# Performance work log

Hardware: AMD Instinct MI355X
Metric: run time of the kernel (lower is better)

Reference implementation:

```python
import jax, jax.numpy as jnp
import numpy as np

NEG_SLOPE = 0.2  # PyG GATConv default leaky_relu slope

def _glorot(key, shape):
    fan_in, fan_out = shape[0], shape[1]
    lim = jnp.sqrt(6.0 / (fan_in + fan_out))
    return jax.random.uniform(key, shape, jnp.float32, -lim, lim)

def setup_inputs() -> dict:
    key = jax.random.key(0)
    ks = jax.random.split(key, 16)
    N, E, S = 20000, 640000, 32
    in_dim, hid, out = 384, 128, 64
    inp = {
        'persona_x': jax.random.normal(ks[0], (N, in_dim), jnp.float32),
        'persona_edge_index': jax.random.randint(ks[1], (2, E), 0, N, jnp.int64),
        'story_x': jax.random.normal(ks[2], (S, N, in_dim), jnp.float32),
        'story_edge_index': jax.random.randint(ks[3], (S, 2, E), 0, N, jnp.int64),
    }
    # persona GAT params
    inp['p_W1'] = _glorot(ks[4], (in_dim, hid)); inp['p_a1'] = _glorot(ks[5], (2 * hid, 1)).reshape(2 * hid)
    inp['p_b1'] = jnp.zeros((hid,), jnp.float32)
    inp['p_W2'] = _glorot(ks[6], (hid, out)); inp['p_a2'] = _glorot(ks[7], (2 * out, 1)).reshape(2 * out)
    inp['p_b2'] = jnp.zeros((out,), jnp.float32)
    # story GAT params
    inp['s_W1'] = _glorot(ks[8], (in_dim, hid)); inp['s_a1'] = _glorot(ks[9], (2 * hid, 1)).reshape(2 * hid)
    inp['s_b1'] = jnp.zeros((hid,), jnp.float32)
    inp['s_W2'] = _glorot(ks[10], (hid, out)); inp['s_a2'] = _glorot(ks[11], (2 * out, 1)).reshape(2 * out)
    inp['s_b2'] = jnp.zeros((out,), jnp.float32)
    inp['temperature'] = jnp.asarray(0.07, jnp.float32)
    return inp

def gat_conv(x, edge_index, W, a, b):
    # x: [N, F_in], edge_index: [2, E] (row 0 = src, row 1 = dst), PyG GATConv heads=1
    N = x.shape[0]
    h = x @ W  # [N, F_out]
    src, dst = edge_index[0], edge_index[1]
    F_out = h.shape[1]
    # PyG adds self-loops by default
    loops = jnp.arange(N, dtype=src.dtype)
    src = jnp.concatenate([src, loops]); dst = jnp.concatenate([dst, loops])
    h_src = h[src]  # [E+N, F_out]
    h_dst = h[dst]
    # alpha = leaky_relu(a_src . h_src + a_dst . h_dst)
    a_src, a_dst = a[:F_out], a[F_out:]
    e = jax.nn.leaky_relu(h_src @ a_src + h_dst @ a_dst, NEG_SLOPE)  # [E+N]
    # segment softmax over destination nodes
    e_max = jax.ops.segment_max(e, dst, num_segments=N)
    e_exp = jnp.exp(e - e_max[dst])
    denom = jax.ops.segment_sum(e_exp, dst, num_segments=N)
    alpha = e_exp / (denom[dst] + 1e-16)
    out = jax.ops.segment_sum(h_src * alpha[:, None], dst, num_segments=N)
    return out + b

def persona_gnn(x, edge_index, W1, a1, b1, W2, a2, b2):
    h = jax.nn.relu(gat_conv(x, edge_index, W1, a1, b1))
    h = gat_conv(h, edge_index, W2, a2, b2)
    return h.mean(axis=0)  # [out_dim]

def reference(persona_x, persona_edge_index, story_x, story_edge_index,
              p_W1, p_a1, p_b1, p_W2, p_a2, p_b2,
              s_W1, s_a1, s_b1, s_W2, s_a2, s_b2, temperature):
    persona_emb = persona_gnn(persona_x, persona_edge_index, p_W1, p_a1, p_b1, p_W2, p_a2, p_b2)
    story_embs = jax.vmap(lambda x, ei: persona_gnn(x, ei, s_W1, s_a1, s_b1, s_W2, s_a2, s_b2))(
        story_x, story_edge_index)  # [S, out_dim]
    p = persona_emb / jnp.linalg.norm(persona_emb)
    s = story_embs / jnp.linalg.norm(story_embs, axis=1, keepdims=True)
    return (s @ p) / temperature  # [S]
```

## Files before the change

### kernel.cpp

```cpp
#include <hip/hip_runtime.h>
#include <cstdio>
#include <cstdint>

constexpr int N_NODES = 20000;
constexpr int E_EDGES = 640000;
constexpr int S_STORIES = 32;
constexpr int G_TOT = 33;
constexpr int IN_DIM = 384;
constexpr int HID = 128;
constexpr int F_OUT = 64;
constexpr float NEG_SLOPE = 0.2f;

constexpr int EPB = 8192;
constexpr int NB = (E_EDGES + EPB - 1) / EPB;
constexpr int NBUCK = (N_NODES + 63) / 64;

typedef short short8 __attribute__((ext_vector_type(8)));
typedef float f32x4 __attribute__((ext_vector_type(4)));

__device__ __forceinline__ float leaky(float x) { return x > 0.f ? x : NEG_SLOPE * x; }

__device__ __forceinline__ uint32_t f2bf(float x) {
    uint32_t u = __builtin_bit_cast(uint32_t, x);
    return (u + 0x7fffu + ((u >> 16) & 1u)) >> 16;
}
__device__ __forceinline__ uint32_t pk2(float lo, float hi) { return (f2bf(hi) << 16) | f2bf(lo); }
__device__ __forceinline__ float bflo(uint32_t u) { return __builtin_bit_cast(float, u << 16); }
__device__ __forceinline__ float bfhi(uint32_t u) { return __builtin_bit_cast(float, u & 0xffff0000u); }

__global__ void zero_kernel(float* __restrict__ b, size_t nb) {
    size_t i = (size_t)blockIdx.x * blockDim.x + threadIdx.x;
    if (i < nb) b[i] = 0.f;
}

__global__ __launch_bounds__(256) void csr_count(const int* __restrict__ pei, const int* __restrict__ sei,
                                                 unsigned* __restrict__ C) {
    int blk = blockIdx.x;
    int g = blk / NB, k = blk - g * NB;
    const int* ei = (g == 0) ? pei : sei + (size_t)(g - 1) * 2 * E_EDGES;
    const int* dstp = ei + E_EDGES;
    int lo = k * EPB, hi = min(lo + EPB, E_EDGES);
    __shared__ unsigned cnt[NBUCK];
    for (int i = threadIdx.x; i < NBUCK; i += 256) cnt[i] = 0;
    __syncthreads();
    for (int i = lo + threadIdx.x; i < hi; i += 256)
        atomicAdd(&cnt[dstp[i] >> 6], 1u);
    __syncthreads();
    unsigned* Cb = C + ((size_t)g * NB + k) * NBUCK;
    for (int i = threadIdx.x; i < NBUCK; i += 256) Cb[i] = cnt[i];
}

__global__ __launch_bounds__(512) void csr_scan(unsigned* __restrict__ C, unsigned* __restrict__ BB) {
    int g = blockIdx.x;
    __shared__ unsigned tot[NBUCK + 1];
    unsigned* Cg = C + (size_t)g * NB * NBUCK;
    for (int b = threadIdx.x; b < NBUCK; b += 512) {
        unsigned s = 0;
        for (int k = 0; k < NB; ++k) s += Cg[(size_t)k * NBUCK + b];
        tot[b] = s;
    }
    __syncthreads();
    if (threadIdx.x == 0) {
        unsigned run = 0;
        for (int b = 0; b < NBUCK; ++b) { unsigned t = tot[b]; tot[b] = run; run += t; }
        tot[NBUCK] = run;
    }
    __syncthreads();
    for (int b = threadIdx.x; b <= NBUCK; b += 512) BB[(size_t)g * (NBUCK + 1) + b] = tot[b];
    for (int b = threadIdx.x; b < NBUCK; b += 512) {
        unsigned run = tot[b];
        for (int k = 0; k < NB; ++k) {
            unsigned t = Cg[(size_t)k * NBUCK + b];
            Cg[(size_t)k * NBUCK + b] = run;
            run += t;
        }
    }
}

__global__ __launch_bounds__(256) void csr_bucket(const int* __restrict__ pei, const int* __restrict__ sei,
                                                  const unsigned* __restrict__ C, unsigned* __restrict__ tmp) {
    int blk = blockIdx.x;
    int g = blk / NB, k = blk - g * NB;
    const int* ei = (g == 0) ? pei : sei + (size_t)(g - 1) * 2 * E_EDGES;
    int lo = k * EPB, hi = min(lo + EPB, E_EDGES);
    __shared__ unsigned off[NBUCK];
    const unsigned* Cb = C + ((size_t)g * NB + k) * NBUCK;
    for (int i = threadIdx.x; i < NBUCK; i += 256) off[i] = Cb[i];
    __syncthreads();
    unsigned* tg = tmp + (size_t)g * E_EDGES;
    for (int i = lo + threadIdx.x; i < hi; i += 256) {
        int s = ei[i], d = ei[E_EDGES + i];
        unsigned r = atomicAdd(&off[d >> 6], 1u);
        tg[r] = ((unsigned)(d & 63) << 15) | (unsigned)s;
    }
}

__global__ __launch_bounds__(256) void csr_fine(const unsigned* __restrict__ tmp, const unsigned* __restrict__ BB,
                                                int* __restrict__ row, int* __restrict__ csr_src) {
    int blk = blockIdx.x;
    int g = blk / NBUCK, b = blk - g * NBUCK;
    unsigned lo = BB[(size_t)g * (NBUCK + 1) + b];
    unsigned hi = BB[(size_t)g * (NBUCK + 1) + b + 1];
    __shared__ unsigned cnt[64];
    __shared__ unsigned pos[64];
    if (threadIdx.x < 64) cnt[threadIdx.x] = 0;
    __syncthreads();
    const unsigned* tg = tmp + (size_t)g * E_EDGES;
    for (unsigned i = lo + threadIdx.x; i < hi; i += 256)
        atomicAdd(&cnt[(tg[i] >> 15) & 63], 1u);
    __syncthreads();
    if (threadIdx.x < 64) {
        unsigned v = cnt[threadIdx.x];
        unsigned inc = v;
#pragma unroll
        for (int o = 1; o < 64; o <<= 1) {
            unsigned u = __shfl_up(inc, o);
            if ((int)threadIdx.x >= o) inc += u;
        }
        unsigned e = inc - v;
        pos[threadIdx.x] = lo + e;
        int n = b * 64 + (int)threadIdx.x;
        if (n <= N_NODES) row[(size_t)g * (N_NODES + 1) + n] = (int)(lo + e);
    }
    __syncthreads();
    for (unsigned i = lo + threadIdx.x; i < hi; i += 256) {
        unsigned v = tg[i];
        unsigned r = atomicAdd(&pos[(v >> 15) & 63], 1u);
        csr_src[(size_t)g * E_EDGES + r] = (int)(v & 0x7fffu);
    }
}

__global__ void wprep_kernel(const float* __restrict__ pW1, const float* __restrict__ sW1,
                             const float* __restrict__ pW2, const float* __restrict__ sW2,
                             short* __restrict__ w1t, short* __restrict__ w2t) {
    constexpr int N1 = 2 * HID * IN_DIM;
    constexpr int N2 = 2 * F_OUT * HID;
    int idx = blockIdx.x * 256 + threadIdx.x;
    if (idx < N1) {
        int t = idx / (HID * IN_DIM);
        int r = idx % (HID * IN_DIM);
        int col = r / IN_DIM, k = r % IN_DIM;
        const float* W = t ? sW1 : pW1;
        float v = W[(size_t)k * HID + col];
        uint32_t hi = f2bf(v);
        float fhi = __builtin_bit_cast(float, hi << 16);
        w1t[idx]      = (short)hi;
        w1t[idx + N1] = (short)f2bf(v - fhi);
    } else if (idx < N1 + N2) {
        int j = idx - N1;
        int t = j / (F_OUT * HID);
        int r = j % (F_OUT * HID);
        int col = r / HID, k = r % HID;
        const float* W = t ? sW2 : pW2;
        float v = W[(size_t)k * F_OUT + col];
        uint32_t hi = f2bf(v);
        float fhi = __builtin_bit_cast(float, hi << 16);
        w2t[j]      = (short)hi;
        w2t[j + N2] = (short)f2bf(v - fhi);
    }
}

template<int KDIM, int NCOL, bool CVT>
__global__ __launch_bounds__(256) void mm_mfma(const void* __restrict__ pXv, const void* __restrict__ sXv,
                                               const short* __restrict__ wt,
                                               uint16_t* __restrict__ outb) {
    constexpr int BPG = (N_NODES + 127) / 128;
    constexpr int NT = NCOL / 16;
    int g = blockIdx.x / BPG;
    int brow = (blockIdx.x % BPG) * 128;
    const short* wtg = wt + (g ? (size_t)NCOL * KDIM : 0);
    __shared__ __align__(16) short As[128 * 40];
    __shared__ __align__(16) short Bh[NCOL * 40];
    __shared__ __align__(16) short Bl[NCOL * 40];
    int tid = threadIdx.x;
    int w = tid >> 6, l = tid & 63;
    int lr = l & 15, kq = l >> 4;
    f32x4 acc[2][NT] = {};
    for (int k0 = 0; k0 < KDIM; k0 += 32) {
        if (CVT) {
            const float* X = (g == 0) ? (const float*)pXv
                                      : (const float*)sXv + (size_t)(g - 1) * N_NODES * KDIM;
#pragma unroll
            for (int i = 0; i < 4; ++i) {
                int v = tid + i * 256;
                int r = v >> 3, q = v & 7;
                float4 xv = make_float4(0.f, 0.f, 0.f, 0.f);
                if (brow + r < N_NODES)
                    xv = *(const float4*)(X + (size_t)(brow + r) * KDIM + k0 + q * 4);
                uint2 pkd; pkd.x = pk2(xv.x, xv.y); pkd.y = pk2(xv.z, xv.w);
                *(uint2*)(As + r * 40 + q * 4) = pkd;
            }
        } else {
            const uint16_t* X = (g == 0) ? (const uint16_t*)pXv
                                         : (const uint16_t*)sXv + (size_t)(g - 1) * N_NODES * KDIM;
#pragma unroll
            for (int i = 0; i < 2; ++i) {
                int v = tid + i * 256;
                int r = v >> 2, q = v & 3;
                uint4 xv = make_uint4(0u, 0u, 0u, 0u);
                if (brow + r < N_NODES)
                    xv = *(const uint4*)(X + (size_t)(brow + r) * KDIM + k0 + q * 8);
                *(uint4*)(As + r * 40 + q * 8) = xv;
            }
        }
        for (int v = tid; v < NCOL * 4; v += 256) {
            int r = v >> 2, q = v & 3;
            const short* srcp = wtg + (size_t)r * KDIM + k0 + q * 8;
            *(uint4*)(Bh + r * 40 + q * 8) = *(const uint4*)srcp;
            *(uint4*)(Bl + r * 40 + q * 8) = *(const uint4*)(srcp + (size_t)2 * NCOL * KDIM);
        }
        __syncthreads();
        short8 a0 = *(const short8*)(As + (w * 32 + lr) * 40 + kq * 8);
        short8 a1 = *(const short8*)(As + (w * 32 + 16 + lr) * 40 + kq * 8);
#pragma unroll
        for (int ct = 0; ct < NT; ++ct) {
            short8 bh = *(const short8*)(Bh + (ct * 16 + lr) * 40 + kq * 8);
            short8 bl = *(const short8*)(Bl + (ct * 16 + lr) * 40 + kq * 8);
            acc[0][ct] = __builtin_amdgcn_mfma_f32_16x16x32_bf16(a0, bh, acc[0][ct], 0, 0, 0);
            acc[0][ct] = __builtin_amdgcn_mfma_f32_16x16x32_bf16(a0, bl, acc[0][ct], 0, 0, 0);
            acc[1][ct] = __builtin_amdgcn_mfma_f32_16x16x32_bf16(a1, bh, acc[1][ct], 0, 0, 0);
            acc[1][ct] = __builtin_amdgcn_mfma_f32_16x16x32_bf16(a1, bl, acc[1][ct], 0, 0, 0);
        }
        __syncthreads();
    }
#pragma unroll
    for (int rt = 0; rt < 2; ++rt) {
#pragma unroll
        for (int ct = 0; ct < NT; ++ct) {
#pragma unroll
            for (int i = 0; i < 4; ++i) {
                int node = brow + w * 32 + rt * 16 + kq * 4 + i;
                if (node < N_NODES)
                    outb[((size_t)g * N_NODES + node) * NCOL + ct * 16 + lr] = (uint16_t)f2bf(acc[rt][ct][i]);
            }
        }
    }
}

__global__ __launch_bounds__(256) void asad128_kernel(const uint32_t* __restrict__ hb,
                                                      const float* __restrict__ pa, const float* __restrict__ sa,
                                                      float* __restrict__ as_, float* __restrict__ ad_) {
    int wid = (blockIdx.x * 256 + threadIdx.x) >> 6;
    int lane = threadIdx.x & 63;
    if (wid >= G_TOT * N_NODES) return;
    int g = wid / N_NODES;
    const float* a = (g == 0) ? pa : sa;
    uint32_t hv = hb[(size_t)wid * 64 + lane];
    float h0 = bflo(hv), h1 = bfhi(hv);
    float2 a_s = *(const float2*)(a + 2 * lane);
    float2 a_d = *(const float2*)(a + 128 + 2 * lane);
    float s = h0 * a_s.x + h1 * a_s.y;
    float d = h0 * a_d.x + h1 * a_d.y;
#pragma unroll
    for (int off = 32; off; off >>= 1) { s += __shfl_xor(s, off); d += __shfl_xor(d, off); }
    if (lane == 0) { as_[wid] = s; ad_[wid] = d; }
}

__global__ __launch_bounds__(256) void asad64_kernel(const uint32_t* __restrict__ hb,
                                                     const float* __restrict__ pa, const float* __restrict__ sa,
                                                     float* __restrict__ as_, float* __restrict__ ad_) {
    int wid = (blockIdx.x * 256 + threadIdx.x) >> 6;
    int lane = threadIdx.x & 63;
    if (wid >= G_TOT * N_NODES) return;
    int g = wid / N_NODES;
    const float* a = (g == 0) ? pa : sa;
    const uint16_t* hr = (const uint16_t*)(hb + (size_t)wid * 32);
    float h = __builtin_bit_cast(float, (uint32_t)hr[lane] << 16);
    float s = h * a[lane];
    float d = h * a[64 + lane];
#pragma unroll
    for (int off = 32; off; off >>= 1) { s += __shfl_xor(s, off); d += __shfl_xor(d, off); }
    if (lane == 0) { as_[wid] = s; ad_[wid] = d; }
}

__global__ __launch_bounds__(256) void agg128_kernel(const uint32_t* __restrict__ hb,
                                                     const float* __restrict__ as_, const float* __restrict__ ad_,
                                                     const int* __restrict__ row, const int* __restrict__ csr_src,
                                                     const float* __restrict__ pb, const float* __restrict__ sb,
                                                     uint32_t* __restrict__ h1p) {
    int node = blockIdx.x * 4 + (threadIdx.x >> 6);
    int g = node / N_NODES;
    int n = node - g * N_NODES;
    int lane = threadIdx.x & 63;
    int start = row[(size_t)g * (N_NODES + 1) + n];
    int end   = row[(size_t)g * (N_NODES + 1) + n + 1];
    const int* src = csr_src + (size_t)g * E_EDGES;
    const float* asg = as_ + (size_t)g * N_NODES;
    const uint32_t* hg = hb + (size_t)g * N_NODES * 64;
    float ad_d = ad_[node];
    float e_self = leaky(asg[n] + ad_d);
    int grp = lane >> 4;
    int f = lane & 15;
    const uint32_t* hf = hg + f * 4;
    float m = e_self, denomp = 0.f;
    float a0 = 0.f, a1 = 0.f, a2 = 0.f, a3 = 0.f, a4 = 0.f, a5 = 0.f, a6 = 0.f, a7 = 0.f;
    for (int j0 = start; j0 < end; j0 += 64) {
        int j = j0 + lane;
        float e = -3.0e38f; int s0 = 0;
        if (j < end) { s0 = src[j]; e = leaky(asg[s0] + ad_d); }
        float cmax = e;
#pragma unroll
        for (int off = 32; off; off >>= 1) cmax = fmaxf(cmax, __shfl_xor(cmax, off));
        if (cmax > m) {
            float sc = __expf(m - cmax);
            denomp *= sc;
            a0 *= sc; a1 *= sc; a2 *= sc; a3 *= sc; a4 *= sc; a5 *= sc; a6 *= sc; a7 *= sc;
            m = cmax;
        }
        float w0 = (j < end) ? __expf(e - m) : 0.f;
        denomp += w0;
        int cnt = min(64, end - j0);
        for (int t = 0; t < cnt; t += 8) {
            float w_[2]; int s_[2];
#pragma unroll
            for (int u = 0; u < 2; ++u) {
                int tt = t + u * 4 + grp;
                w_[u] = __shfl(w0, tt);
                s_[u] = __shfl(s0, tt);
            }
            uint4 hv_[2];
#pragma unroll
            for (int u = 0; u < 2; ++u)
                hv_[u] = *(const uint4*)(hf + (size_t)s_[u] * 64);
#pragma unroll
            for (int u = 0; u < 2; ++u) {
                float w = w_[u]; uint4 hv = hv_[u];
                a0 += w * bflo(hv.x); a1 += w * bfhi(hv.x);
                a2 += w * bflo(hv.y); a3 += w * bfhi(hv.y);
                a4 += w * bflo(hv.z); a5 += w * bfhi(hv.z);
                a6 += w * bflo(hv.w); a7 += w * bfhi(hv.w);
            }
        }
    }
#pragma unroll
    for (int off = 32; off; off >>= 1) denomp += __shfl_xor(denomp, off);
#pragma unroll
    for (int off = 16; off <= 32; off <<= 1) {
        a0 += __shfl_xor(a0, off); a1 += __shfl_xor(a1, off);
        a2 += __shfl_xor(a2, off); a3 += __shfl_xor(a3, off);
        a4 += __shfl_xor(a4, off); a5 += __shfl_xor(a5, off);
        a6 += __shfl_xor(a6, off); a7 += __shfl_xor(a7, off);
    }
    if (lane < 16) {
        float wself = __expf(e_self - m);
        float inv = 1.f / (denomp + wself + 1e-16f);
        uint4 hv = *(const uint4*)(hg + (size_t)n * 64 + lane * 4);
        const float* b = (g == 0) ? pb : sb;
        float4 b0 = *(const float4*)(b + lane * 8);
        float4 b1 = *(const float4*)(b + lane * 8 + 4);
        float o0 = fmaxf((a0 + wself * bflo(hv.x)) * inv + b0.x, 0.f);
        float o1 = fmaxf((a1 + wself * bfhi(hv.x)) * inv + b0.y, 0.f);
        float o2 = fmaxf((a2 + wself * bflo(hv.y)) * inv + b0.z, 0.f);
        float o3 = fmaxf((a3 + wself * bfhi(hv.y)) * inv + b0.w, 0.f);
        float o4 = fmaxf((a4 + wself * bflo(hv.z)) * inv + b1.x, 0.f);
        float o5 = fmaxf((a5 + wself * bfhi(hv.z)) * inv + b1.y, 0.f);
        float o6 = fmaxf((a6 + wself * bflo(hv.w)) * inv + b1.z, 0.f);
        float o7 = fmaxf((a7 + wself * bfhi(hv.w)) * inv + b1.w, 0.f);
        uint4 o; o.x = pk2(o0, o1); o.y = pk2(o2, o3); o.z = pk2(o4, o5); o.w = pk2(o6, o7);
        *(uint4*)(h1p + (size_t)node * 64 + lane * 4) = o;
    }
}

__global__ __launch_bounds__(256) void agg64_kernel(const uint32_t* __restrict__ hb,
                                                    const float* __restrict__ as_, const float* __restrict__ ad_,
                                                    const int* __restrict__ row, const int* __restrict__ csr_src,
                                                    const float* __restrict__ pb, const float* __restrict__ sb,
                                                    float* __restrict__ outp) {
    int node = blockIdx.x * 4 + (threadIdx.x >> 6);
    int g = node / N_NODES;
    int n = node - g * N_NODES;
    int lane = threadIdx.x & 63;
    int start = row[(size_t)g * (N_NODES + 1) + n];
    int end   = row[(size_t)g * (N_NODES + 1) + n + 1];
    const int* src = csr_src + (size_t)g * E_EDGES;
    const float* asg = as_ + (size_t)g * N_NODES;
    const uint32_t* hg = hb + (size_t)g * N_NODES * 32;
    float ad_d = ad_[node];
    float e_self = leaky(asg[n] + ad_d);
    int grp = lane >> 4;
    int f = lane & 15;
    const uint32_t* hf = hg + f * 2;
    float m = e_self, denomp = 0.f;
    float a0 = 0.f, a1 = 0.f, a2 = 0.f, a3 = 0.f;
    for (int j0 = start; j0 < end; j0 += 64) {
        int j = j0 + lane;
        float e = -3.0e38f; int s0 = 0;
        if (j < end) { s0 = src[j]; e = leaky(asg[s0] + ad_d); }
        float cmax = e;
#pragma unroll
        for (int off = 32; off; off >>= 1) cmax = fmaxf(cmax, __shfl_xor(cmax, off));
        if (cmax > m) {
            float sc = __expf(m - cmax);
            denomp *= sc;
            a0 *= sc; a1 *= sc; a2 *= sc; a3 *= sc;
            m = cmax;
        }
        float w0 = (j < end) ? __expf(e - m) : 0.f;
        denomp += w0;
        int cnt = min(64, end - j0);
        for (int t = 0; t < cnt; t += 16) {
            float w_[4]; int s_[4];
#pragma unroll
            for (int u = 0; u < 4; ++u) {
                int tt = t + u * 4 + grp;
                w_[u] = __shfl(w0, tt);
                s_[u] = __shfl(s0, tt);
            }
            uint2 hv_[4];
#pragma unroll
            for (int u = 0; u < 4; ++u)
                hv_[u] = *(const uint2*)(hf + (size_t)s_[u] * 32);
#pragma unroll
            for (int u = 0; u < 4; ++u) {
                float w = w_[u]; uint2 hv = hv_[u];
                a0 += w * bflo(hv.x); a1 += w * bfhi(hv.x);
                a2 += w * bflo(hv.y); a3 += w * bfhi(hv.y);
            }
        }
    }
#pragma unroll
    for (int off = 32; off; off >>= 1) denomp += __shfl_xor(denomp, off);
#pragma unroll
    for (int off = 16; off <= 32; off <<= 1) {
        a0 += __shfl_xor(a0, off); a1 += __shfl_xor(a1, off);
        a2 += __shfl_xor(a2, off); a3 += __shfl_xor(a3, off);
    }
    if (lane < 16) {
        float wself = __expf(e_self - m);
        float inv = 1.f / (denomp + wself + 1e-16f);
        uint2 hv = *(const uint2*)(hg + (size_t)n * 32 + lane * 2);
        const float* b = (g == 0) ? pb : sb;
        float4 bv = *(const float4*)(b + lane * 4);
        float4 o;
        o.x = (a0 + wself * bflo(hv.x)) * inv + bv.x;
        o.y = (a1 + wself * bfhi(hv.x)) * inv + bv.y;
        o.z = (a2 + wself * bflo(hv.y)) * inv + bv.z;
        o.w = (a3 + wself * bfhi(hv.y)) * inv + bv.w;
        *(float4*)(outp + (size_t)node * 64 + lane * 4) = o;
    }
}

__global__ __launch_bounds__(256) void mean_kernel(const float* __restrict__ out2, float* __restrict__ emb) {
    constexpr int CH = 32;
    int g = blockIdx.x / CH, chunk = blockIdx.x % CH;
    int f = threadIdx.x & 63, sub = threadIdx.x >> 6;
    float acc = 0.f;
    for (int n = chunk * 4 + sub; n < N_NODES; n += CH * 4)
        acc += out2[((size_t)g * N_NODES + n) * 64 + f];
    __shared__ float red[256];
    red[threadIdx.x] = acc;
    __syncthreads();
    if (sub == 0) {
        float s = red[f] + red[64 + f] + red[128 + f] + red[192 + f];
        atomicAdd(&emb[g * 64 + f], s * (1.f / N_NODES));
    }
}

__global__ __launch_bounds__(64) void final_kernel(const float* __restrict__ emb,
                                                   const float* __restrict__ temp, float* __restrict__ out) {
    int lane = threadIdx.x;
    float pe = emb[lane];
    float pp = pe * pe;
#pragma unroll
    for (int off = 32; off; off >>= 1) pp += __shfl_xor(pp, off);
    float t = temp[0];
    float pn = sqrtf(pp);
    for (int s_i = 0; s_i < S_STORIES; ++s_i) {
        float se = emb[(1 + s_i) * 64 + lane];
        float ss = se * se;
        float dt = se * pe;
#pragma unroll
        for (int off = 32; off; off >>= 1) { ss += __shfl_xor(ss, off); dt += __shfl_xor(dt, off); }
        if (lane == 0) out[s_i] = dt / (sqrtf(ss) * pn * t);
    }
}

extern "C" void kernel_launch(void* const* d_in, const int* in_sizes, int n_in,
                              void* d_out, int out_size, void* d_ws, size_t ws_size,
                              hipStream_t stream) {
    const float* persona_x = (const float*)d_in[0];
    const int*   pei       = (const int*)d_in[1];
    const float* story_x   = (const float*)d_in[2];
    const int*   sei       = (const int*)d_in[3];
    const float* p_W1 = (const float*)d_in[4];
    const float* p_a1 = (const float*)d_in[5];
    const float* p_b1 = (const float*)d_in[6];
    const float* p_W2 = (const float*)d_in[7];
    const float* p_a2 = (const float*)d_in[8];
    const float* p_b2 = (const float*)d_in[9];
    const float* s_W1 = (const float*)d_in[10];
    const float* s_a1 = (const float*)d_in[11];
    const float* s_b1 = (const float*)d_in[12];
    const float* s_W2 = (const float*)d_in[13];
    const float* s_a2 = (const float*)d_in[14];
    const float* s_b2 = (const float*)d_in[15];
    const float* temp = (const float*)d_in[16];
    float* out = (float*)d_out;

    char* ws = (char*)d_ws;
    size_t off = 0;
    auto alloc = [&](size_t bytes) { char* p = ws + off; off += (bytes + 255) & ~(size_t)255; return p; };
    uint32_t* hb1  = (uint32_t*)alloc((size_t)G_TOT * N_NODES * 64 * 4);
    uint32_t* h1p  = (uint32_t*)alloc((size_t)G_TOT * N_NODES * 64 * 4);
    uint32_t* hb2  = (uint32_t*)alloc((size_t)G_TOT * N_NODES * 32 * 4);
    float* as_     = (float*)alloc((size_t)G_TOT * N_NODES * 4);
    float* ad_     = (float*)alloc((size_t)G_TOT * N_NODES * 4);
    int*   csr_row = (int*)  alloc((size_t)G_TOT * (N_NODES + 1) * 4);
    int*   csr_src = (int*)  alloc((size_t)G_TOT * E_EDGES * 4);
    float* emb     = (float*)alloc((size_t)G_TOT * 64 * 4);
    short* w1t     = (short*)alloc((size_t)2 * 2 * HID * IN_DIM * 2);
    short* w2t     = (short*)alloc((size_t)2 * 2 * F_OUT * HID * 2);
    if (off > ws_size) {
        fprintf(stderr, "kernel_launch: ws too small: need %zu have %zu\n", off, ws_size);
        return;
    }
    unsigned* tmp = (unsigned*)hb1;
    unsigned* C   = (unsigned*)h1p;
    unsigned* BB  = (unsigned*)h1p + (size_t)G_TOT * NB * NBUCK;
    float* out2   = (float*)hb1;

    constexpr int BPG = (N_NODES + 127) / 128;
    const int NODE_BLOCKS = G_TOT * N_NODES / 4;

    zero_kernel<<<(G_TOT * 64 + 255) / 256, 256, 0, stream>>>(emb, (size_t)G_TOT * 64);
    wprep_kernel<<<(2 * HID * IN_DIM + 2 * F_OUT * HID + 255) / 256, 256, 0, stream>>>(p_W1, s_W1, p_W2, s_W2, w1t, w2t);
    csr_count <<<G_TOT * NB, 256, 0, stream>>>(pei, sei, C);
    csr_scan  <<<G_TOT, 512, 0, stream>>>(C, BB);
    csr_bucket<<<G_TOT * NB, 256, 0, stream>>>(pei, sei, C, tmp);
    csr_fine  <<<G_TOT * NBUCK, 256, 0, stream>>>(tmp, BB, csr_row, csr_src);

    mm_mfma<IN_DIM, HID, true><<<G_TOT * BPG, 256, 0, stream>>>(persona_x, story_x, w1t, (uint16_t*)hb1);
    asad128_kernel<<<(G_TOT * N_NODES + 3) / 4, 256, 0, stream>>>(hb1, p_a1, s_a1, as_, ad_);
    agg128_kernel<<<NODE_BLOCKS, 256, 0, stream>>>(hb1, as_, ad_, csr_row, csr_src, p_b1, s_b1, h1p);

    const uint16_t* h1p16 = (const uint16_t*)h1p;
    mm_mfma<HID, F_OUT, false><<<G_TOT * BPG, 256, 0, stream>>>(h1p16, h1p16 + (size_t)N_NODES * HID, w2t, (uint16_t*)hb2);
    asad64_kernel<<<(G_TOT * N_NODES + 3) / 4, 256, 0, stream>>>(hb2, p_a2, s_a2, as_, ad_);
    agg64_kernel<<<NODE_BLOCKS, 256, 0, stream>>>(hb2, as_, ad_, csr_row, csr_src, p_b2, s_b2, out2);

    mean_kernel<<<G_TOT * 32, 256, 0, stream>>>(out2, emb);
    final_kernel<<<1, 64, 0, stream>>>(emb, temp, out);
}
```

Measured before the change: 2.192 ms.

## Fuse attention score projections into matmul epilogue and mean into aggregation

The per-node attention dot products (a_src·h, a_dst·h) are now computed inside the MFMA matmul epilogue from the fp32 accumulators with a 16-lane shuffle reduction, removing the two separate asad kernels that re-read the projected features. The layer-2 aggregation kernel now reduces its four nodes per block in shared memory and atomically adds into the per-graph mean embedding, eliminating the fp32 output buffer and the separate mean kernel. This removes large intermediate reads and writes and kernel launches, but introduces many contended atomics on a small set of addresses and slightly changes numerics (scores from unrounded fp32 values).

```diff
diff --git a/kernel.cpp b/kernel.cpp
--- a/kernel.cpp
+++ b/kernel.cpp
@@ -163,7 +163,9 @@
 template<int KDIM, int NCOL, bool CVT>
 __global__ __launch_bounds__(256) void mm_mfma(const void* __restrict__ pXv, const void* __restrict__ sXv,
                                                const short* __restrict__ wt,
-                                               uint16_t* __restrict__ outb) {
+                                               const float* __restrict__ pa, const float* __restrict__ sa,
+                                               uint16_t* __restrict__ outb,
+                                               float* __restrict__ as_, float* __restrict__ ad_) {
     constexpr int BPG = (N_NODES + 127) / 128;
     constexpr int NT = NCOL / 16;
     int g = blockIdx.x / BPG;
@@ -223,54 +225,35 @@
         }
         __syncthreads();
     }
+    const float* av = (g == 0) ? pa : sa;
+    float aS[NT], aD[NT];
+#pragma unroll
+    for (int ct = 0; ct < NT; ++ct) {
+        aS[ct] = av[ct * 16 + lr];
+        aD[ct] = av[NCOL + ct * 16 + lr];
+    }
 #pragma unroll
     for (int rt = 0; rt < 2; ++rt) {
 #pragma unroll
-        for (int ct = 0; ct < NT; ++ct) {
-#pragma unroll
-            for (int i = 0; i < 4; ++i) {
-                int node = brow + w * 32 + rt * 16 + kq * 4 + i;
+        for (int i = 0; i < 4; ++i) {
+            int node = brow + w * 32 + rt * 16 + kq * 4 + i;
+            float s = 0.f, d = 0.f;
+#pragma unroll
+            for (int ct = 0; ct < NT; ++ct) {
+                float h = acc[rt][ct][i];
+                s += h * aS[ct];
+                d += h * aD[ct];
                 if (node < N_NODES)
-                    outb[((size_t)g * N_NODES + node) * NCOL + ct * 16 + lr] = (uint16_t)f2bf(acc[rt][ct][i]);
-            }
-        }
-    }
-}
-
-__global__ __launch_bounds__(256) void asad128_kernel(const uint32_t* __restrict__ hb,
-                                                      const float* __restrict__ pa, const float* __restrict__ sa,
-                                                      float* __restrict__ as_, float* __restrict__ ad_) {
-    int wid = (blockIdx.x * 256 + threadIdx.x) >> 6;
-    int lane = threadIdx.x & 63;
-    if (wid >= G_TOT * N_NODES) return;
-    int g = wid / N_NODES;
-    const float* a = (g == 0) ? pa : sa;
-    uint32_t hv = hb[(size_t)wid * 64 + lane];
-    float h0 = bflo(hv), h1 = bfhi(hv);
-    float2 a_s = *(const float2*)(a + 2 * lane);
-    float2 a_d = *(const float2*)(a + 128 + 2 * lane);
-    float s = h0 * a_s.x + h1 * a_s.y;
-    float d = h0 * a_d.x + h1 * a_d.y;
-#pragma unroll
-    for (int off = 32; off; off >>= 1) { s += __shfl_xor(s, off); d += __shfl_xor(d, off); }
-    if (lane == 0) { as_[wid] = s; ad_[wid] = d; }
-}
-
-__global__ __launch_bounds__(256) void asad64_kernel(const uint32_t* __restrict__ hb,
-                                                     const float* __restrict__ pa, const float* __restrict__ sa,
-                                                     float* __restrict__ as_, float* __restrict__ ad_) {
-    int wid = (blockIdx.x * 256 + threadIdx.x) >> 6;
-    int lane = threadIdx.x & 63;
-    if (wid >= G_TOT * N_NODES) return;
-    int g = wid / N_NODES;
-    const float* a = (g == 0) ? pa : sa;
-    const uint16_t* hr = (const uint16_t*)(hb + (size_t)wid * 32);
-    float h = __builtin_bit_cast(float, (uint32_t)hr[lane] << 16);
-    float s = h * a[lane];
-    float d = h * a[64 + lane];
-#pragma unroll
-    for (int off = 32; off; off >>= 1) { s += __shfl_xor(s, off); d += __shfl_xor(d, off); }
-    if (lane == 0) { as_[wid] = s; ad_[wid] = d; }
+                    outb[((size_t)g * N_NODES + node) * NCOL + ct * 16 + lr] = (uint16_t)f2bf(h);
+            }
+#pragma unroll
+            for (int off = 1; off < 16; off <<= 1) { s += __shfl_xor(s, off); d += __shfl_xor(d, off); }
+            if (lr == 0 && node < N_NODES) {
+                as_[(size_t)g * N_NODES + node] = s;
+                ad_[(size_t)g * N_NODES + node] = d;
+            }
+        }
+    }
 }
 
 __global__ __launch_bounds__(256) void agg128_kernel(const uint32_t* __restrict__ hb,
@@ -365,8 +348,9 @@
                                                     const float* __restrict__ as_, const float* __restrict__ ad_,
                                                     const int* __restrict__ row, const int* __restrict__ csr_src,
                                                     const float* __restrict__ pb, const float* __restrict__ sb,
-                                                    float* __restrict__ outp) {
-    int node = blockIdx.x * 4 + (threadIdx.x >> 6);
+                                                    float* __restrict__ emb) {
+    int widx = threadIdx.x >> 6;
+    int node = blockIdx.x * 4 + widx;
     int g = node / N_NODES;
     int n = node - g * N_NODES;
     int lane = threadIdx.x & 63;
@@ -425,6 +409,7 @@
         a0 += __shfl_xor(a0, off); a1 += __shfl_xor(a1, off);
         a2 += __shfl_xor(a2, off); a3 += __shfl_xor(a3, off);
     }
+    __shared__ float red[4][64];
     if (lane < 16) {
         float wself = __expf(e_self - m);
         float inv = 1.f / (denomp + wself + 1e-16f);
@@ -436,23 +421,12 @@
         o.y = (a1 + wself * bfhi(hv.x)) * inv + bv.y;
         o.z = (a2 + wself * bflo(hv.y)) * inv + bv.z;
         o.w = (a3 + wself * bfhi(hv.y)) * inv + bv.w;
-        *(float4*)(outp + (size_t)node * 64 + lane * 4) = o;
-    }
-}
-
-__global__ __launch_bounds__(256) void mean_kernel(const float* __restrict__ out2, float* __restrict__ emb) {
-    constexpr int CH = 32;
-    int g = blockIdx.x / CH, chunk = blockIdx.x % CH;
-    int f = threadIdx.x & 63, sub = threadIdx.x >> 6;
-    float acc = 0.f;
-    for (int n = chunk * 4 + sub; n < N_NODES; n += CH * 4)
-        acc += out2[((size_t)g * N_NODES + n) * 64 + f];
-    __shared__ float red[256];
-    red[threadIdx.x] = acc;
-    __syncthreads();
-    if (sub == 0) {
-        float s = red[f] + red[64 + f] + red[128 + f] + red[192 + f];
-        atomicAdd(&emb[g * 64 + f], s * (1.f / N_NODES));
+        *(float4*)(&red[widx][lane * 4]) = o;
+    }
+    __syncthreads();
+    if (threadIdx.x < 64) {
+        float s = red[0][threadIdx.x] + red[1][threadIdx.x] + red[2][threadIdx.x] + red[3][threadIdx.x];
+        atomicAdd(&emb[g * 64 + threadIdx.x], s * (1.f / N_NODES));
     }
 }
 
@@ -517,7 +491,6 @@
     unsigned* tmp = (unsigned*)hb1;
     unsigned* C   = (unsigned*)h1p;
     unsigned* BB  = (unsigned*)h1p + (size_t)G_TOT * NB * NBUCK;
-    float* out2   = (float*)hb1;
 
     constexpr int BPG = (N_NODES + 127) / 128;
     const int NODE_BLOCKS = G_TOT * N_NODES / 4;
@@ -529,15 +502,14 @@
     csr_bucket<<<G_TOT * NB, 256, 0, stream>>>(pei, sei, C, tmp);
     csr_fine  <<<G_TOT * NBUCK, 256, 0, stream>>>(tmp, BB, csr_row, csr_src);
 
-    mm_mfma<IN_DIM, HID, true><<<G_TOT * BPG, 256, 0, stream>>>(persona_x, story_x, w1t, (uint16_t*)hb1);
-    asad128_kernel<<<(G_TOT * N_NODES + 3) / 4, 256, 0, stream>>>(hb1, p_a1, s_a1, as_, ad_);
+    mm_mfma<IN_DIM, HID, true><<<G_TOT * BPG, 256, 0, stream>>>(persona_x, story_x, w1t, p_a1, s_a1,
+                                                                (uint16_t*)hb1, as_, ad_);
     agg128_kernel<<<NODE_BLOCKS, 256, 0, stream>>>(hb1, as_, ad_, csr_row, csr_src, p_b1, s_b1, h1p);
 
     const uint16_t* h1p16 = (const uint16_t*)h1p;
-    mm_mfma<HID, F_OUT, false><<<G_TOT * BPG, 256, 0, stream>>>(h1p16, h1p16 + (size_t)N_NODES * HID, w2t, (uint16_t*)hb2);
-    asad64_kernel<<<(G_TOT * N_NODES + 3) / 4, 256, 0, stream>>>(hb2, p_a2, s_a2, as_, ad_);
-    agg64_kernel<<<NODE_BLOCKS, 256, 0, stream>>>(hb2, as_, ad_, csr_row, csr_src, p_b2, s_b2, out2);
-
-    mean_kernel<<<G_TOT * 32, 256, 0, stream>>>(out2, emb);
+    mm_mfma<HID, F_OUT, false><<<G_TOT * BPG, 256, 0, stream>>>(h1p16, h1p16 + (size_t)N_NODES * HID, w2t, p_a2, s_a2,
+                                                                (uint16_t*)hb2, as_, ad_);
+    agg64_kernel<<<NODE_BLOCKS, 256, 0, stream>>>(hb2, as_, ad_, csr_row, csr_src, p_b2, s_b2, emb);
+
     final_kernel<<<1, 64, 0, stream>>>(emb, temp, out);
 }
```

Measured after the change: 2.403 ms. 1.1x slower.
